# Optimization experiments

Hardware: AMD Instinct MI355X
Metric: run time of the kernel (lower is better)

The kernel has to match this reference:

```python
import jax, jax.numpy as jnp
import numpy as np

B, N, F, K = 16384, 64, 128, 64


def setup_inputs() -> dict:
    key = jax.random.key(0)
    kx, kd = jax.random.split(key)
    x = jax.random.normal(kx, (B, F), dtype=jnp.float32)
    D = jax.random.normal(kd, (N, F, K), dtype=jnp.float32)  # per-cluster factor dictionaries
    return {"x": x, "D": D}


def reference(x, D):
    # --- assignment step (torch.no_grad in original) ---
    # Dtx[n,b,j] = sum_i D[n,i,j] * x[b,i]
    Dtx = jnp.einsum('nij,bi->nbj', D, x)                      # [N,B,K]
    # per-cluster (D^T D)^{-1}, batched inverse over the cluster axis
    DTD = jnp.einsum('nij,nik->njk', D, D)                     # [N,K,K]
    DTD_inv = jnp.linalg.inv(DTD)                              # [N,K,K]
    Cs = jnp.einsum('nbj,nkj->nbk', Dtx, DTD_inv)              # [N,B,K]
    x_hat = jnp.einsum('nij,nbj->nbi', D, Cs)                  # [N,B,F]
    # nearest-subspace assignment per sample
    label = jnp.argmin(jnp.linalg.norm(x_hat - x[None], axis=-1), axis=0)  # [B] int
    C = Cs[label, jnp.arange(x.shape[0])]                      # [B,K] gather per sample
    # --- reconstruction loss: sum_i || x[i] - D[label[i]] @ C[i] ||^2 ---
    x_rec = jnp.einsum('bik,bk->bi', D[label], C)              # grouped gather + matmul
    se_loss = jnp.sum(jnp.square(x - x_rec))
    return se_loss, label
```

## Files before the change

kernel.cpp:

```cpp
#include <hip/hip_runtime.h>
#include <hip/hip_bf16.h>

#define B_N 16384
#define TAU 0.25f
#define GS 68
#define YS 132
#define DS 68

typedef float f32x4 __attribute__((ext_vector_type(4)));
typedef short s16x8 __attribute__((ext_vector_type(8)));

__device__ __forceinline__ void gl_lds16(const void* g, void* l) {
    __builtin_amdgcn_global_load_lds(
        (const __attribute__((address_space(1))) void*)g,
        (__attribute__((address_space(3))) void*)l, 16, 0, 0);
}

__device__ __forceinline__ unsigned short bf16_bits(float v) {
    __hip_bfloat16 h = __float2bfloat16(v);
    return *reinterpret_cast<unsigned short*>(&h);
}

__device__ __forceinline__ float readlane_f(float v, int l) {
    return __int_as_float(__builtin_amdgcn_readlane(__float_as_int(v), l));
}

__global__ __launch_bounds__(512) void prep_convert(const float* __restrict__ x,
                                                    const float* __restrict__ D,
                                                    unsigned short* __restrict__ xh,
                                                    float* __restrict__ nrm,
                                                    float* __restrict__ Qg,
                                                    unsigned short* __restrict__ Bht,
                                                    float* __restrict__ out) {
    const int t = threadIdx.x;

    if (blockIdx.x >= 64) {
        const int gid = (blockIdx.x - 64) * 512 + t;
        if (gid == 0) out[0] = 0.0f;
        const size_t base = (size_t)gid * 32;
        float s = 0.0f;
        #pragma unroll
        for (int c = 0; c < 8; ++c) {
            const f32x4 v = ((const f32x4*)(x + base))[c];
            s += v.x * v.x + v.y * v.y + v.z * v.z + v.w * v.w;
            ushort4 h;
            h.x = bf16_bits(v.x); h.y = bf16_bits(v.y);
            h.z = bf16_bits(v.z); h.w = bf16_bits(v.w);
            ((ushort4*)(xh + base))[c] = h;
        }
        s += __shfl_xor(s, 1, 64);
        s += __shfl_xor(s, 2, 64);
        if ((gid & 3) == 0) nrm[gid >> 2] = s;
        return;
    }

    __shared__ float Y[64 * YS];
    __shared__ __align__(16) float Dl[128 * DS];
    __shared__ __align__(16) float G[64 * GS + 64];
    __shared__ __align__(16) float Lti[8 * 8 * 8];
    const int n = blockIdx.x;
    const float* Dn = D + (size_t)n * 8192;

    for (int e4 = t; e4 < 2048; e4 += 512) {
        const int c = e4 >> 4, j4 = (e4 & 15) * 4;
        const f32x4 v = ((const f32x4*)Dn)[e4];
        *(f32x4*)&Dl[c * DS + j4] = v;
        Y[(j4 + 0) * YS + c] = v.x;
        Y[(j4 + 1) * YS + c] = v.y;
        Y[(j4 + 2) * YS + c] = v.z;
        Y[(j4 + 3) * YS + c] = v.w;
    }
    __syncthreads();

    {
        const int h = t >> 8;
        const int a0 = (t & 15) * 4, b0 = ((t >> 4) & 15) * 4;
        const int i0 = h * 64;
        float acc[4][4] = {};
        #pragma unroll 4
        for (int i = i0; i < i0 + 64; ++i) {
            const f32x4 av = *(const f32x4*)&Dl[i * DS + a0];
            const f32x4 bv = *(const f32x4*)&Dl[i * DS + b0];
            const float aa[4] = {av.x, av.y, av.z, av.w};
            const float bb[4] = {bv.x, bv.y, bv.z, bv.w};
            #pragma unroll
            for (int p = 0; p < 4; ++p)
                #pragma unroll
                for (int q = 0; q < 4; ++q) acc[p][q] = fmaf(aa[p], bb[q], acc[p][q]);
        }
        if (h == 0) {
            #pragma unroll
            for (int p = 0; p < 4; ++p)
                #pragma unroll
                for (int q = 0; q < 4; ++q) G[(a0 + p) * GS + b0 + q] = acc[p][q];
        }
        __syncthreads();
        if (h == 1) {
            #pragma unroll
            for (int p = 0; p < 4; ++p)
                #pragma unroll
                for (int q = 0; q < 4; ++q) G[(a0 + p) * GS + b0 + q] += acc[p][q];
        }
    }
    __syncthreads();

    #pragma unroll
    for (int p8 = 0; p8 < 8; ++p8) {
        const int pb = p8 * 8;
        if (t < 64) {
            const int lane = t;
            const f32x4 v0 = *(const f32x4*)&G[lane * GS + pb];
            const f32x4 v1 = *(const f32x4*)&G[lane * GS + pb + 4];
            float g[8] = {v0.x, v0.y, v0.z, v0.w, v1.x, v1.y, v1.z, v1.w};
            #pragma unroll
            for (int kk = 0; kk < 8; ++kk) {
                const int k = pb + kk;
                const float dk = readlane_f(g[kk], k);
                const float rinv = 1.0f / sqrtf(dk);
                const float lik = g[kk] * rinv;
                g[kk] = lik;
                if (lane == 0) G[64 * GS + k] = rinv;
                #pragma unroll
                for (int jj = kk + 1; jj < 8; ++jj) {
                    const float ljk = readlane_f(lik, pb + jj);
                    g[jj] -= lik * ljk;
                }
            }
            *(f32x4*)&G[lane * GS + pb]     = (f32x4){g[0], g[1], g[2], g[3]};
            *(f32x4*)&G[lane * GS + pb + 4] = (f32x4){g[4], g[5], g[6], g[7]};
        }
        __syncthreads();
        const int base = pb + 8;
        if (base < 64) {
            for (int i = base + (t >> 5); i < 64; i += 16) {
                const f32x4 Li0 = *(const f32x4*)&G[i * GS + pb];
                const f32x4 Li1 = *(const f32x4*)&G[i * GS + pb + 4];
                for (int j = base + (t & 31); j < 64; j += 32) {
                    const f32x4 Lj0 = *(const f32x4*)&G[j * GS + pb];
                    const f32x4 Lj1 = *(const f32x4*)&G[j * GS + pb + 4];
                    float s = G[i * GS + j];
                    s -= Li0.x * Lj0.x + Li0.y * Lj0.y + Li0.z * Lj0.z + Li0.w * Lj0.w;
                    s -= Li1.x * Lj1.x + Li1.y * Lj1.y + Li1.z * Lj1.z + Li1.w * Lj1.w;
                    G[i * GS + j] = s;
                }
            }
        }
        __syncthreads();
    }

    if (t < 64) {
        const int bi = t >> 3, c = t & 7;
        const int base = bi * 8;
        float m[8];
        #pragma unroll
        for (int r = 0; r < 8; ++r) {
            float s = (r == c) ? 1.0f : 0.0f;
            #pragma unroll
            for (int k = 0; k < r; ++k)
                s -= G[(base + r) * GS + base + k] * m[k];
            m[r] = s * G[64 * GS + base + r];
        }
        #pragma unroll
        for (int r = 0; r < 8; ++r) Lti[(base + r) * 8 + c] = m[r];
    }
    __syncthreads();

    {
        const int j = t >> 3, r = t & 7, jb = j >> 3;
        const float rinvj = G[64 * GS + j];
        for (int m8 = 0; m8 < 8; ++m8) {
            if (m8 >= jb) {
                const int g = m8 * 8 + r;
                float wv = (g == j) ? 1.0f : 0.0f;
                if (m8 > jb) {
                    #pragma unroll
                    for (int kk = 0; kk < 8; ++kk) {
                        const int gp = jb * 8 + kk;
                        const float liv = (gp > j) ? G[j * GS + gp]
                                         : ((gp == j) ? rinvj : 0.0f);
                        wv -= G[g * GS + gp] * liv;
                    }
                    for (int mm = jb + 1; mm < m8; ++mm) {
                        const f32x4 Lg0 = *(const f32x4*)&G[g * GS + mm * 8];
                        const f32x4 Lg1 = *(const f32x4*)&G[g * GS + mm * 8 + 4];
                        const f32x4 Mv0 = *(const f32x4*)&G[j * GS + mm * 8];
                        const f32x4 Mv1 = *(const f32x4*)&G[j * GS + mm * 8 + 4];
                        wv = fmaf(-Lg0.x, Mv0.x, wv);
                        wv = fmaf(-Lg0.y, Mv0.y, wv);
                        wv = fmaf(-Lg0.z, Mv0.z, wv);
                        wv = fmaf(-Lg0.w, Mv0.w, wv);
                        wv = fmaf(-Lg1.x, Mv1.x, wv);
                        wv = fmaf(-Lg1.y, Mv1.y, wv);
                        wv = fmaf(-Lg1.z, Mv1.z, wv);
                        wv = fmaf(-Lg1.w, Mv1.w, wv);
                    }
                }
                float z = 0.0f;
                #pragma unroll
                for (int rp = 0; rp < 8; ++rp) {
                    const float wrp = __shfl(wv, (t & 56) | rp, 64);
                    z = fmaf(Lti[g * 8 + rp], wrp, z);
                }
                if (g > j) G[j * GS + g] = z;
            }
            __syncthreads();
        }
    }

    {
        const int jj = t >> 5;
        const int jz = (jj & 1) ? (15 - (jj >> 1)) : (jj >> 1);
        const int j0 = jz * 4, c0 = (t & 31) * 4;
        const f32x4 rv4 = *(const f32x4*)&G[64 * GS + j0];
        float acc[4][4] = {};
        #pragma unroll 4
        for (int k = 0; k < j0; ++k) {
            const f32x4 lv = *(const f32x4*)&G[k * GS + j0];
            const f32x4 yv = *(const f32x4*)&Y[k * YS + c0];
            #pragma unroll
            for (int ej = 0; ej < 4; ++ej)
                #pragma unroll
                for (int ec = 0; ec < 4; ++ec)
                    acc[ej][ec] = fmaf(lv[ej], yv[ec], acc[ej][ec]);
        }
        #pragma unroll
        for (int kt = 0; kt < 4; ++kt) {
            const int k = j0 + kt;
            const f32x4 lq = *(const f32x4*)&G[k * GS + j0];
            const f32x4 yv = *(const f32x4*)&Y[k * YS + c0];
            #pragma unroll
            for (int ej = 0; ej < 4; ++ej) {
                const int jjj = j0 + ej;
                const float lsel = (jjj > k) ? lq[ej] : ((jjj == k) ? rv4[ej] : 0.0f);
                #pragma unroll
                for (int ec = 0; ec < 4; ++ec)
                    acc[ej][ec] = fmaf(lsel, yv[ec], acc[ej][ec]);
            }
        }
        #pragma unroll
        for (int ec = 0; ec < 4; ++ec) {
            *(f32x4*)&Qg[(size_t)n * 8192 + (c0 + ec) * 64 + j0] =
                (f32x4){acc[0][ec], acc[1][ec], acc[2][ec], acc[3][ec]};
        }
        #pragma unroll
        for (int ej = 0; ej < 4; ++ej) {
            ushort4 h;
            h.x = bf16_bits(acc[ej][0]); h.y = bf16_bits(acc[ej][1]);
            h.z = bf16_bits(acc[ej][2]); h.w = bf16_bits(acc[ej][3]);
            *(ushort4*)&Bht[((size_t)n * 64 + j0 + ej) * 128 + c0] = h;
        }
    }
}

__global__ __launch_bounds__(256) void gemm_scores(const unsigned short* __restrict__ xh,
                                                   const unsigned short* __restrict__ Bht,
                                                   float* __restrict__ S) {
    __shared__ unsigned short ldsA[128 * 128];
    __shared__ unsigned short ldsB[64 * 128];
    const int t = threadIdx.x, w = t >> 6, lane = t & 63;
    const int m0 = blockIdx.x * 128;
    const int n0 = blockIdx.y * 8;
    const int lm = lane & 15, lg = lane >> 4;

    {
        const int rl = lane >> 4, p = lane & 15;
        #pragma unroll
        for (int q = 0; q < 8; ++q) {
            const int row = w * 32 + q * 4 + rl;
            const int c = p ^ (row & 15);
            gl_lds16(xh + (size_t)(m0 + row) * 128 + c * 8,
                     &ldsA[(w * 32 + q * 4) * 128]);
        }
        #pragma unroll
        for (int q = 0; q < 4; ++q) {
            const int row = w * 16 + q * 4 + rl;
            const int c = p ^ (row & 15);
            gl_lds16(Bht + ((size_t)n0 * 64 + row) * 128 + c * 8,
                     &ldsB[(w * 16 + q * 4) * 128]);
        }
    }
    __syncthreads();

    s16x8 af[2][4];
    #pragma unroll
    for (int mt = 0; mt < 2; ++mt) {
        const int r = w * 32 + mt * 16 + lm;
        #pragma unroll
        for (int ks = 0; ks < 4; ++ks) {
            const int p = (ks * 4 + lg) ^ (r & 15);
            af[mt][ks] = *(const s16x8*)&ldsA[r * 128 + p * 8];
        }
    }

    #pragma unroll 1
    for (int it = 0; it < 8; ++it) {
        const int nc = n0 + it;

        s16x8 bf[4][4];
        #pragma unroll
        for (int nt = 0; nt < 4; ++nt) {
            const int r = nt * 16 + lm;
            #pragma unroll
            for (int ks = 0; ks < 4; ++ks) {
                const int p = (ks * 4 + lg) ^ (r & 15);
                bf[nt][ks] = *(const s16x8*)&ldsB[r * 128 + p * 8];
            }
        }
        __syncthreads();

        if (it < 7) {
            const int rl = lane >> 4, p = lane & 15;
            #pragma unroll
            for (int q = 0; q < 4; ++q) {
                const int row = w * 16 + q * 4 + rl;
                const int c = p ^ (row & 15);
                gl_lds16(Bht + ((size_t)(nc + 1) * 64 + row) * 128 + c * 8,
                         &ldsB[(w * 16 + q * 4) * 128]);
            }
        }

        #pragma unroll
        for (int mt = 0; mt < 2; ++mt) {
            f32x4 acc[4];
            #pragma unroll
            for (int nt = 0; nt < 4; ++nt) acc[nt] = (f32x4){0.f, 0.f, 0.f, 0.f};
            #pragma unroll
            for (int ks = 0; ks < 4; ++ks)
                #pragma unroll
                for (int nt = 0; nt < 4; ++nt)
                    acc[nt] = __builtin_amdgcn_mfma_f32_16x16x32_bf16(
                        af[mt][ks], bf[nt][ks], acc[nt], 0, 0, 0);
            #pragma unroll
            for (int rg = 0; rg < 4; ++rg) {
                float p = 0.0f;
                #pragma unroll
                for (int nt = 0; nt < 4; ++nt) {
                    const float v = acc[nt][rg];
                    p += v * v;
                }
                p += __shfl_xor(p, 1, 64);
                p += __shfl_xor(p, 2, 64);
                p += __shfl_xor(p, 4, 64);
                p += __shfl_xor(p, 8, 64);
                if (lm == 0)
                    S[(size_t)nc * B_N + m0 + w * 32 + mt * 16 + lg * 4 + rg] = p;
            }
        }
        __syncthreads();
    }
}

__global__ __launch_bounds__(256) void argmax_rescore(const float* __restrict__ Sa,
                                                      const float* __restrict__ nrm,
                                                      const float* __restrict__ x,
                                                      const float* __restrict__ Qg,
                                                      float* __restrict__ out) {
    __shared__ float tile[32 * 65];
    __shared__ int sflags[32];
    __shared__ int scnt;
    __shared__ float ssum;
    __shared__ float scorr[4];
    const int t = threadIdx.x, w = t >> 6, lane = t & 63;
    const int b0 = blockIdx.x * 32;
    if (t == 0) scnt = 0;

    for (int e = t; e < 512; e += 256) {
        const int n = e >> 3, c4 = e & 7;
        const f32x4 v = *(const f32x4*)&Sa[(size_t)n * B_N + b0 + c4 * 4];
        tile[(c4 * 4 + 0) * 65 + n] = v.x;
        tile[(c4 * 4 + 1) * 65 + n] = v.y;
        tile[(c4 * 4 + 2) * 65 + n] = v.z;
        tile[(c4 * 4 + 3) * 65 + n] = v.w;
    }
    __syncthreads();

    if (t < 32) {
        float v1 = -1e30f, v2 = -1e30f;
        int n1 = 0;
        for (int n = 0; n < 64; ++n) {
            const float v = tile[t * 65 + n];
            if (v > v1) { v2 = v1; v1 = v; n1 = n; }
            else v2 = fmaxf(v2, v);
        }
        out[1 + b0 + t] = (float)n1;
        if (v1 - v2 < TAU) { const int i = atomicAdd(&scnt, 1); sflags[i] = t; }
        float err = nrm[b0 + t] - v1;
        err += __shfl_xor(err, 1, 64);
        err += __shfl_xor(err, 2, 64);
        err += __shfl_xor(err, 4, 64);
        err += __shfl_xor(err, 8, 64);
        err += __shfl_xor(err, 16, 64);
        if (t == 0) ssum = err;
    }
    if (lane == 0) scorr[w] = 0.0f;
    __syncthreads();

    const int nf = scnt;
    float corr = 0.0f;
    for (int f = w; f < nf; f += 4) {
        const int s = sflags[f];
        const int b2 = b0 + s;
        const float v = tile[s * 65 + lane];
        float vm = v;
        for (int off = 32; off; off >>= 1) vm = fmaxf(vm, __shfl_xor(vm, off, 64));
        unsigned long long mask = __ballot((vm - v) < TAU);
        float best = -1e30f;
        int bn = 0;
        while (mask) {
            const int nn = (int)__builtin_ctzll(mask);
            mask &= mask - 1;
            const float* Qn = Qg + (size_t)nn * 8192;
            const float* xb = x + (size_t)b2 * 128;
            float d0 = 0.0f, d1 = 0.0f, d2 = 0.0f, d3 = 0.0f;
            #pragma unroll
            for (int i = 0; i < 128; i += 4) {
                d0 = fmaf(Qn[(i + 0) * 64 + lane], xb[i + 0], d0);
                d1 = fmaf(Qn[(i + 1) * 64 + lane], xb[i + 1], d1);
                d2 = fmaf(Qn[(i + 2) * 64 + lane], xb[i + 2], d2);
                d3 = fmaf(Qn[(i + 3) * 64 + lane], xb[i + 3], d3);
            }
            const float dot = (d0 + d1) + (d2 + d3);
            float sv = dot * dot;
            for (int off = 32; off; off >>= 1) sv += __shfl_xor(sv, off, 64);
            if (sv > best) { best = sv; bn = nn; }
        }
        if (lane == 0) {
            out[1 + b2] = (float)bn;
            corr += vm - best;
        }
    }
    if (lane == 0 && corr != 0.0f) scorr[w] += corr;
    __syncthreads();
    if (t == 0)
        atomicAdd(out, ssum + scorr[0] + scorr[1] + scorr[2] + scorr[3]);
}

extern "C" void kernel_launch(void* const* d_in, const int* in_sizes, int n_in,
                              void* d_out, int out_size, void* d_ws, size_t ws_size,
                              hipStream_t stream) {
    const float* x = (const float*)d_in[0];
    const float* D = (const float*)d_in[1];
    float* out = (float*)d_out;

    char* ws = (char*)d_ws;
    unsigned short* xh  = (unsigned short*)(ws);
    unsigned short* Bht = (unsigned short*)(ws + (4u << 20));
    float* Qg           = (float*)(ws + (5u << 20));
    float* Sa           = (float*)(ws + (7u << 20));
    float* nrm          = (float*)(ws + (11u << 20));

    prep_convert<<<192, 512, 0, stream>>>(x, D, xh, nrm, Qg, Bht, out);
    gemm_scores<<<dim3(128, 8), 256, 0, stream>>>(xh, Bht, Sa);
    argmax_rescore<<<512, 256, 0, stream>>>(Sa, nrm, x, Qg, out);
}
```

Baseline: 142.4 us.

## Fuse score GEMM with argmax and rescore, keeping scores in LDS

Merges the score GEMM and the argmax/rescore kernel into one kernel. Each block owns 64 samples and loops over all 64 clusters, double-buffering the cluster basis tiles in LDS. The per-sample scores are reduced in shared memory and the running top-2 is tracked on the fly. This removes the global score buffer round trip and one kernel launch. In exchange the grid drops to 256 blocks, which lowers parallelism, and wave 0 does a serial reduction every iteration.

```diff
diff --git a/kernel.cpp b/kernel.cpp
--- a/kernel.cpp
+++ b/kernel.cpp
@@ -252,155 +252,133 @@
     }
 }
 
-__global__ __launch_bounds__(256) void gemm_scores(const unsigned short* __restrict__ xh,
+__global__ __launch_bounds__(256) void gemm_argmax(const unsigned short* __restrict__ xh,
                                                    const unsigned short* __restrict__ Bht,
-                                                   float* __restrict__ S) {
-    __shared__ unsigned short ldsA[128 * 128];
-    __shared__ unsigned short ldsB[64 * 128];
-    const int t = threadIdx.x, w = t >> 6, lane = t & 63;
-    const int m0 = blockIdx.x * 128;
-    const int n0 = blockIdx.y * 8;
-    const int lm = lane & 15, lg = lane >> 4;
-
-    {
-        const int rl = lane >> 4, p = lane & 15;
-        #pragma unroll
-        for (int q = 0; q < 8; ++q) {
-            const int row = w * 32 + q * 4 + rl;
-            const int c = p ^ (row & 15);
-            gl_lds16(xh + (size_t)(m0 + row) * 128 + c * 8,
-                     &ldsA[(w * 32 + q * 4) * 128]);
-        }
-        #pragma unroll
-        for (int q = 0; q < 4; ++q) {
-            const int row = w * 16 + q * 4 + rl;
-            const int c = p ^ (row & 15);
-            gl_lds16(Bht + ((size_t)n0 * 64 + row) * 128 + c * 8,
-                     &ldsB[(w * 16 + q * 4) * 128]);
-        }
-    }
-    __syncthreads();
-
-    s16x8 af[2][4];
-    #pragma unroll
-    for (int mt = 0; mt < 2; ++mt) {
-        const int r = w * 32 + mt * 16 + lm;
-        #pragma unroll
-        for (int ks = 0; ks < 4; ++ks) {
-            const int p = (ks * 4 + lg) ^ (r & 15);
-            af[mt][ks] = *(const s16x8*)&ldsA[r * 128 + p * 8];
-        }
-    }
-
-    #pragma unroll 1
-    for (int it = 0; it < 8; ++it) {
-        const int nc = n0 + it;
-
-        s16x8 bf[4][4];
-        #pragma unroll
-        for (int nt = 0; nt < 4; ++nt) {
-            const int r = nt * 16 + lm;
-            #pragma unroll
-            for (int ks = 0; ks < 4; ++ks) {
-                const int p = (ks * 4 + lg) ^ (r & 15);
-                bf[nt][ks] = *(const s16x8*)&ldsB[r * 128 + p * 8];
-            }
-        }
-        __syncthreads();
-
-        if (it < 7) {
-            const int rl = lane >> 4, p = lane & 15;
-            #pragma unroll
-            for (int q = 0; q < 4; ++q) {
-                const int row = w * 16 + q * 4 + rl;
-                const int c = p ^ (row & 15);
-                gl_lds16(Bht + ((size_t)(nc + 1) * 64 + row) * 128 + c * 8,
-                         &ldsB[(w * 16 + q * 4) * 128]);
-            }
-        }
-
-        #pragma unroll
-        for (int mt = 0; mt < 2; ++mt) {
-            f32x4 acc[4];
-            #pragma unroll
-            for (int nt = 0; nt < 4; ++nt) acc[nt] = (f32x4){0.f, 0.f, 0.f, 0.f};
-            #pragma unroll
-            for (int ks = 0; ks < 4; ++ks)
-                #pragma unroll
-                for (int nt = 0; nt < 4; ++nt)
-                    acc[nt] = __builtin_amdgcn_mfma_f32_16x16x32_bf16(
-                        af[mt][ks], bf[nt][ks], acc[nt], 0, 0, 0);
-            #pragma unroll
-            for (int rg = 0; rg < 4; ++rg) {
-                float p = 0.0f;
-                #pragma unroll
-                for (int nt = 0; nt < 4; ++nt) {
-                    const float v = acc[nt][rg];
-                    p += v * v;
-                }
-                p += __shfl_xor(p, 1, 64);
-                p += __shfl_xor(p, 2, 64);
-                p += __shfl_xor(p, 4, 64);
-                p += __shfl_xor(p, 8, 64);
-                if (lm == 0)
-                    S[(size_t)nc * B_N + m0 + w * 32 + mt * 16 + lg * 4 + rg] = p;
-            }
-        }
-        __syncthreads();
-    }
-}
-
-__global__ __launch_bounds__(256) void argmax_rescore(const float* __restrict__ Sa,
-                                                      const float* __restrict__ nrm,
-                                                      const float* __restrict__ x,
-                                                      const float* __restrict__ Qg,
-                                                      float* __restrict__ out) {
-    __shared__ float tile[32 * 65];
-    __shared__ int sflags[32];
+                                                   const float* __restrict__ nrm,
+                                                   const float* __restrict__ x,
+                                                   const float* __restrict__ Qg,
+                                                   float* __restrict__ out) {
+    __shared__ __align__(16) unsigned short ldsA[64 * 128];
+    __shared__ __align__(16) unsigned short ldsB[2][64 * 128];
+    __shared__ float scL[64 * 65];
+    __shared__ float scPart[2][16][80];
+    __shared__ int sflags[64];
     __shared__ int scnt;
     __shared__ float ssum;
     __shared__ float scorr[4];
     const int t = threadIdx.x, w = t >> 6, lane = t & 63;
-    const int b0 = blockIdx.x * 32;
+    const int m0 = blockIdx.x * 64;
+    const int lm = lane & 15, lg = lane >> 4;
     if (t == 0) scnt = 0;
-
-    for (int e = t; e < 512; e += 256) {
-        const int n = e >> 3, c4 = e & 7;
-        const f32x4 v = *(const f32x4*)&Sa[(size_t)n * B_N + b0 + c4 * 4];
-        tile[(c4 * 4 + 0) * 65 + n] = v.x;
-        tile[(c4 * 4 + 1) * 65 + n] = v.y;
-        tile[(c4 * 4 + 2) * 65 + n] = v.z;
-        tile[(c4 * 4 + 3) * 65 + n] = v.w;
-    }
-    __syncthreads();
-
-    if (t < 32) {
-        float v1 = -1e30f, v2 = -1e30f;
-        int n1 = 0;
-        for (int n = 0; n < 64; ++n) {
-            const float v = tile[t * 65 + n];
-            if (v > v1) { v2 = v1; v1 = v; n1 = n; }
-            else v2 = fmaxf(v2, v);
-        }
-        out[1 + b0 + t] = (float)n1;
-        if (v1 - v2 < TAU) { const int i = atomicAdd(&scnt, 1); sflags[i] = t; }
-        float err = nrm[b0 + t] - v1;
+    if (t < 4) scorr[t] = 0.0f;
+
+    {
+        const int rl = lane >> 4, p = lane & 15;
+        #pragma unroll
+        for (int q = 0; q < 4; ++q) {
+            const int row = w * 16 + q * 4 + rl;
+            const int c = p ^ (row & 15);
+            gl_lds16(xh + (size_t)(m0 + row) * 128 + c * 8,
+                     &ldsA[(w * 16 + q * 4) * 128]);
+        }
+        #pragma unroll
+        for (int q = 0; q < 4; ++q) {
+            const int row = w * 16 + q * 4 + rl;
+            const int c = p ^ (row & 15);
+            gl_lds16(Bht + (size_t)row * 128 + c * 8,
+                     &ldsB[0][(w * 16 + q * 4) * 128]);
+        }
+    }
+    __syncthreads();
+
+    s16x8 bf[4][4];
+    #pragma unroll
+    for (int st = 0; st < 4; ++st) {
+        const int r = st * 16 + lm;
+        #pragma unroll
+        for (int ks = 0; ks < 4; ++ks) {
+            const int p = (ks * 4 + lg) ^ (r & 15);
+            bf[st][ks] = *(const s16x8*)&ldsA[r * 128 + p * 8];
+        }
+    }
+
+    float v1 = -1e30f, v2 = -1e30f;
+    int n1 = 0;
+
+    #pragma unroll 1
+    for (int it = 0; it < 64; ++it) {
+        const int cur = it & 1;
+
+        s16x8 af[4];
+        {
+            const int r = w * 16 + lm;
+            #pragma unroll
+            for (int ks = 0; ks < 4; ++ks) {
+                const int p = (ks * 4 + lg) ^ (r & 15);
+                af[ks] = *(const s16x8*)&ldsB[cur][r * 128 + p * 8];
+            }
+        }
+
+        if (it < 63) {
+            const int rl = lane >> 4, p = lane & 15;
+            #pragma unroll
+            for (int q = 0; q < 4; ++q) {
+                const int row = w * 16 + q * 4 + rl;
+                const int c = p ^ (row & 15);
+                gl_lds16(Bht + ((size_t)(it + 1) * 64 + row) * 128 + c * 8,
+                         &ldsB[cur ^ 1][(w * 16 + q * 4) * 128]);
+            }
+        }
+
+        #pragma unroll
+        for (int st = 0; st < 4; ++st) {
+            f32x4 acc = (f32x4){0.f, 0.f, 0.f, 0.f};
+            #pragma unroll
+            for (int ks = 0; ks < 4; ++ks)
+                acc = __builtin_amdgcn_mfma_f32_16x16x32_bf16(af[ks], bf[st][ks], acc, 0, 0, 0);
+            float q = acc[0] * acc[0];
+            q = fmaf(acc[1], acc[1], q);
+            q = fmaf(acc[2], acc[2], q);
+            q = fmaf(acc[3], acc[3], q);
+            scPart[cur][w * 4 + lg][st * 16 + lm] = q;
+        }
+
+        if (it > 0 && w == 0) {
+            const int pb = cur ^ 1;
+            float s = scPart[pb][0][lane];
+            #pragma unroll
+            for (int idx = 1; idx < 16; ++idx) s += scPart[pb][idx][lane];
+            scL[lane * 65 + (it - 1)] = s;
+            if (s > v1) { v2 = v1; v1 = s; n1 = it - 1; } else v2 = fmaxf(v2, s);
+        }
+        __syncthreads();
+    }
+
+    if (w == 0) {
+        float s = scPart[1][0][lane];
+        #pragma unroll
+        for (int idx = 1; idx < 16; ++idx) s += scPart[1][idx][lane];
+        scL[lane * 65 + 63] = s;
+        if (s > v1) { v2 = v1; v1 = s; n1 = 63; } else v2 = fmaxf(v2, s);
+        out[1 + m0 + lane] = (float)n1;
+        if (v1 - v2 < TAU) { const int i = atomicAdd(&scnt, 1); sflags[i] = lane; }
+        float err = nrm[m0 + lane] - v1;
         err += __shfl_xor(err, 1, 64);
         err += __shfl_xor(err, 2, 64);
         err += __shfl_xor(err, 4, 64);
         err += __shfl_xor(err, 8, 64);
         err += __shfl_xor(err, 16, 64);
-        if (t == 0) ssum = err;
-    }
-    if (lane == 0) scorr[w] = 0.0f;
+        err += __shfl_xor(err, 32, 64);
+        if (lane == 0) ssum = err;
+    }
     __syncthreads();
 
     const int nf = scnt;
     float corr = 0.0f;
     for (int f = w; f < nf; f += 4) {
         const int s = sflags[f];
-        const int b2 = b0 + s;
-        const float v = tile[s * 65 + lane];
+        const int b2 = m0 + s;
+        const float v = scL[s * 65 + lane];
         float vm = v;
         for (int off = 32; off; off >>= 1) vm = fmaxf(vm, __shfl_xor(vm, off, 64));
         unsigned long long mask = __ballot((vm - v) < TAU);
@@ -446,10 +424,8 @@
     unsigned short* xh  = (unsigned short*)(ws);
     unsigned short* Bht = (unsigned short*)(ws + (4u << 20));
     float* Qg           = (float*)(ws + (5u << 20));
-    float* Sa           = (float*)(ws + (7u << 20));
     float* nrm          = (float*)(ws + (11u << 20));
 
     prep_convert<<<192, 512, 0, stream>>>(x, D, xh, nrm, Qg, Bht, out);
-    gemm_scores<<<dim3(128, 8), 256, 0, stream>>>(xh, Bht, Sa);
-    argmax_rescore<<<512, 256, 0, stream>>>(Sa, nrm, x, Qg, out);
-}
+    gemm_argmax<<<256, 256, 0, stream>>>(xh, Bht, nrm, x, Qg, out);
+}
```

Measured after the change: 138.2 us. 3.0% less time.
